# Kernel tuning notes

Measured on AMD Instinct MI355X. Metric: run time of the kernel, lower is better.

Reference implementation:

```python
import jax, jax.numpy as jnp
import numpy as np

NEG_INF = -1e9

def apply_rope(x, positions, head_dim, theta):
    # x: [B, S, H, Dh]; positions: [S] int32
    half = head_dim // 2
    fraction = (2.0 / head_dim) * jnp.arange(half, dtype=jnp.float32)  # [Dh/2]
    timescale = theta ** fraction
    angle = positions.astype(jnp.float32)[:, None] / timescale  # [S, Dh/2]
    sin = jnp.sin(angle)[None, :, None, :]  # [1,S,1,Dh/2]
    cos = jnp.cos(angle)[None, :, None, :]
    x1, x2 = jnp.split(x, 2, axis=-1)
    out = jnp.concatenate([x1 * cos - x2 * sin, x2 * cos + x1 * sin], axis=-1)
    return out.astype(x.dtype)

def setup_inputs() -> dict:
    key = jax.random.key(0)
    B, S, D = 2, 2048, 2048
    Q, N, H = 16, 4, 128
    ks = jax.random.split(key, 5)
    scale = 1.0 / np.sqrt(D)
    return {
        "x": jax.random.normal(ks[0], (B, S, D), dtype=jnp.float32),
        "positions": jnp.arange(S, dtype=jnp.int32),
        "Wq": jax.random.normal(ks[1], (Q, D, H), dtype=jnp.float32) * scale,
        "Wk": jax.random.normal(ks[2], (N, D, H), dtype=jnp.float32) * scale,
        "Wv": jax.random.normal(ks[3], (N, D, H), dtype=jnp.float32) * scale,
        "Wo": jax.random.normal(ks[4], (Q, H, D), dtype=jnp.float32) * scale,
    }

def reference(x, positions, Wq, Wk, Wv, Wo):
    head_dim = Wq.shape[-1]
    theta = 10000.0
    head_repeats = Wq.shape[0] // Wk.shape[0]  # GQA repeat factor

    q_BSQH = jnp.einsum('BSD,QDH->BSQH', x, Wq)
    q_BSQH = apply_rope(q_BSQH, positions, head_dim, theta)
    k_BTNH = jnp.einsum('BSD,NDH->BSNH', x, Wk)
    k_BTNH = apply_rope(k_BTNH, positions, head_dim, theta)
    v_BTNH = jnp.einsum('BSD,NDH->BSNH', x, Wv)

    k_BTQH = jnp.repeat(k_BTNH, head_repeats, axis=2)
    v_BTQH = jnp.repeat(v_BTNH, head_repeats, axis=2)

    scores_BQST = jnp.einsum('BSQH,BTQH->BQST', q_BSQH, k_BTQH) / jnp.sqrt(
        jnp.asarray(head_dim, dtype=x.dtype))
    S = q_BSQH.shape[1]
    causal = jnp.tril(jnp.ones((1, 1, S, S), dtype=jnp.bool_))
    scores_BQST = jnp.where(causal, scores_BQST, NEG_INF)
    weights_BQST = jax.nn.softmax(scores_BQST, axis=-1)
    out_BSQH = jnp.einsum('BQST,BTQH->BSQH', weights_BQST, v_BTQH)
    o_BSD = jnp.einsum('BSQH,QHD->BSD', out_BSQH, Wo)
    return o_BSD
```

## Files before the change

kernel.cpp:

```cpp
#include <hip/hip_runtime.h>
#include <math.h>

#define BB 2
#define SS 2048
#define DD 2048
#define QH 16
#define NKV 4
#define HD 128
#define REP 4
#define NEG_INF_F (-1e9f)

typedef __bf16 bfrag __attribute__((ext_vector_type(8)));
typedef float  ffrag __attribute__((ext_vector_type(4)));

__device__ inline unsigned short f2bf(float f) {
    unsigned u = __builtin_bit_cast(unsigned, f);
    u += 0x7fff + ((u >> 16) & 1);
    return (unsigned short)(u >> 16);
}
__device__ inline float bf2f(unsigned short u) {
    unsigned v = (unsigned)u << 16;
    return __builtin_bit_cast(float, v);
}
__device__ inline bfrag ld_frag(const unsigned short* p) {
    uint4 u = *(const uint4*)p;
    return __builtin_bit_cast(bfrag, u);
}
__device__ inline void async16(const void* g, void* l) {
    __builtin_amdgcn_global_load_lds(
        (const __attribute__((address_space(1))) unsigned int*)g,
        (__attribute__((address_space(3))) unsigned int*)l, 16, 0, 0);
}
__device__ inline unsigned pkbf(float a, float b) {
    unsigned short ua = __builtin_bit_cast(unsigned short, (__bf16)a);
    unsigned short ub = __builtin_bit_cast(unsigned short, (__bf16)b);
    return (unsigned)ua | ((unsigned)ub << 16);
}

__global__ void cast_x_kernel(const float* __restrict__ x,
                              unsigned short* __restrict__ xb, int n)
{
    const int i = (blockIdx.x * blockDim.x + threadIdx.x) * 8;
    if (i >= n) return;
    float4 a = *(const float4*)(x + i);
    float4 b = *(const float4*)(x + i + 4);
    unsigned short o[8];
    o[0] = f2bf(a.x); o[1] = f2bf(a.y); o[2] = f2bf(a.z); o[3] = f2bf(a.w);
    o[4] = f2bf(b.x); o[5] = f2bf(b.y); o[6] = f2bf(b.z); o[7] = f2bf(b.w);
    *(uint4*)(xb + i) = *(uint4*)o;
}

__global__ __launch_bounds__(256) void tcast_kernel(
    const float* __restrict__ in, unsigned short* __restrict__ out,
    int R, int C)
{
    __shared__ float tile[32][33];
    const size_t bofs = (size_t)blockIdx.z * R * C;
    in  += bofs;
    out += bofs;
    const int c0 = blockIdx.x * 32, r0 = blockIdx.y * 32;
    const int tx = threadIdx.x & 31, ty = threadIdx.x >> 5;
    #pragma unroll
    for (int k = 0; k < 4; ++k)
        tile[ty + 8 * k][tx] = in[(size_t)(r0 + ty + 8 * k) * C + c0 + tx];
    __syncthreads();
    #pragma unroll
    for (int k = 0; k < 4; ++k)
        out[(size_t)(c0 + ty + 8 * k) * R + r0 + tx] =
            f2bf(tile[tx][ty + 8 * k]);
}

__global__ __launch_bounds__(256) void gemm_bt_kernel(
    const unsigned short* __restrict__ A,
    const unsigned short* __restrict__ Bt,
    unsigned short* __restrict__ q_out, unsigned short* __restrict__ k_out,
    unsigned short* __restrict__ vt_out, float* __restrict__ f_out,
    int mode)
{
    const int m0 = blockIdx.x * 128;
    const int n0 = blockIdx.y * 128;
    const int tid  = threadIdx.x;
    const int w    = tid >> 6, lane = tid & 63;
    const int l16  = lane & 15, quad = lane >> 4;
    const int wm = (w >> 1) * 64, wn = (w & 1) * 64;

    __shared__ unsigned short As[128 * 32];
    __shared__ unsigned short Bs[128 * 32];

    ffrag acc[4][4];
    #pragma unroll
    for (int mi = 0; mi < 4; ++mi)
        #pragma unroll
        for (int ni = 0; ni < 4; ++ni)
            acc[mi][ni] = (ffrag){0.f, 0.f, 0.f, 0.f};

    for (int k0 = 0; k0 < 2048; k0 += 32) {
        __syncthreads();
        #pragma unroll
        for (int j = 0; j < 2; ++j) {
            const int i   = (j * 4 + w) * 64 + lane;
            const int row = i >> 2, seg = i & 3;
            async16(&A [(size_t)(m0 + row) * 2048 + k0 + seg * 8],
                    (char*)As + i * 16);
            async16(&Bt[(size_t)(n0 + row) * 2048 + k0 + seg * 8],
                    (char*)Bs + i * 16);
        }
        __syncthreads();

        bfrag af[4], bfr[4];
        #pragma unroll
        for (int mi = 0; mi < 4; ++mi)
            af[mi] = ld_frag(&As[(wm + mi * 16 + l16) * 32 + quad * 8]);
        #pragma unroll
        for (int ni = 0; ni < 4; ++ni)
            bfr[ni] = ld_frag(&Bs[(wn + ni * 16 + l16) * 32 + quad * 8]);
        #pragma unroll
        for (int mi = 0; mi < 4; ++mi)
            #pragma unroll
            for (int ni = 0; ni < 4; ++ni)
                acc[mi][ni] = __builtin_amdgcn_mfma_f32_16x16x32_bf16(
                    af[mi], bfr[ni], acc[mi][ni], 0, 0, 0);
    }

    if (mode == 0) {
        #pragma unroll
        for (int mi = 0; mi < 4; ++mi)
            #pragma unroll
            for (int ni = 0; ni < 4; ++ni) {
                const int col = n0 + wn + ni * 16 + l16;
                #pragma unroll
                for (int r = 0; r < 4; ++r) {
                    const int row = m0 + wm + mi * 16 + quad * 4 + r;
                    f_out[(size_t)row * 2048 + col] = acc[mi][ni][r];
                }
            }
    } else if (n0 < 2560) {
        unsigned short* dst;
        int colbase, stride;
        if (n0 < 2048)      { dst = q_out; colbase = n0;        stride = 2048; }
        else                { dst = k_out; colbase = n0 - 2048; stride = 512;  }
        #pragma unroll
        for (int mi = 0; mi < 4; ++mi)
            #pragma unroll
            for (int ni = 0; ni < 4; ++ni) {
                const int col = colbase + wn + ni * 16 + l16;
                #pragma unroll
                for (int r = 0; r < 4; ++r) {
                    const int row = m0 + wm + mi * 16 + quad * 4 + r;
                    dst[(size_t)row * stride + col] = f2bf(acc[mi][ni][r]);
                }
            }
    } else {
        const int c3 = n0 - 2560;
        #pragma unroll
        for (int mi = 0; mi < 4; ++mi)
            #pragma unroll
            for (int ni = 0; ni < 4; ++ni) {
                const int col = c3 + wn + ni * 16 + l16;
                const int nh = col >> 7, h = col & 127;
                const int row0 = m0 + wm + mi * 16 + quad * 4;
                const int b = row0 >> 11, s = row0 & 2047;
                unsigned short pk[4];
                #pragma unroll
                for (int r = 0; r < 4; ++r) pk[r] = f2bf(acc[mi][ni][r]);
                *(uint2*)&vt_out[(((size_t)b * NKV + nh) * HD + h) * SS + s] =
                    *(uint2*)pk;
            }
    }
}

__global__ void rope_kernel(unsigned short* __restrict__ q,
                            unsigned short* __restrict__ k,
                            const int* __restrict__ positions)
{
    const int qpairs = BB * SS * QH * 64;
    const int kpairs = BB * SS * NKV * 64;
    int idx = blockIdx.x * blockDim.x + threadIdx.x;
    unsigned short* base;
    int nh;
    if (idx < qpairs) { base = q; nh = QH; }
    else {
        idx -= qpairs;
        if (idx >= kpairs) return;
        base = k; nh = NKV;
    }
    const int hh   = idx & 63;
    const int rest = idx >> 6;
    const int head = rest % nh;
    const int bs   = rest / nh;
    const int s    = bs % SS;

    unsigned short* p = base + ((size_t)bs * nh + head) * HD;
    const float pos = (float)positions[s];
    const float inv_ts = powf(10000.0f, -(float)hh * (1.0f / 64.0f));
    const float angle = pos * inv_ts;
    const float sn = sinf(angle), cs = cosf(angle);
    const float sc_ = (nh == QH) ? 0.08838834764831845f : 1.0f;
    const float x1 = bf2f(p[hh]), x2 = bf2f(p[hh + 64]);
    p[hh]      = f2bf((x1 * cs - x2 * sn) * sc_);
    p[hh + 64] = f2bf((x2 * cs + x1 * sn) * sc_);
}

__global__ __launch_bounds__(256, 2) void attn_kernel(
    const unsigned short* __restrict__ qb,
    const unsigned short* __restrict__ kb,
    const unsigned short* __restrict__ vt,
    unsigned short* __restrict__ o)
{
    const int bh = blockIdx.y;
    const int b  = bh / QH, qh = bh % QH;
    const int n  = qh / REP;

    const int tid  = threadIdx.x;
    const int w    = tid >> 6;
    const int lane = tid & 63;
    const int l16  = lane & 15;
    const int quad = lane >> 4;
    const int sw   = l16 & 7;

    __shared__ unsigned short Ks[2][2][64][64];
    __shared__ unsigned short Vs[2][128][64];
    __shared__ unsigned short Ps[4][16][72];

    const unsigned short* kbase = kb + (size_t)b * (SS * NKV * HD) + n * HD;
    const unsigned short* vbase = vt + ((size_t)b * NKV + n) * HD * SS;

    for (int ph = 0; ph < 2; ++ph) {
        const int tile = ph == 0 ? (31 - (int)blockIdx.x) : (int)blockIdx.x;
        const int s0 = tile * 64;
        const int rbase = s0 + w * 16 + quad * 4;
        const int thr   = w * 16 + l16;

        bfrag qf[4];
        {
            const unsigned short* qp =
                qb + ((size_t)(b * SS + s0 + w * 16 + l16) * QH + qh) * HD
                   + quad * 8;
            #pragma unroll
            for (int c = 0; c < 4; ++c) qf[c] = ld_frag(qp + c * 32);
        }
        ffrag oacc[8];
        #pragma unroll
        for (int t = 0; t < 8; ++t) oacc[t] = (ffrag){0.f, 0.f, 0.f, 0.f};
        float mr = -1e30f, lr = 0.0f;

        #pragma unroll
        for (int j = 0; j < 4; ++j) {
            const int s = j * 256 + tid;
            {   const int cc = s >> 9, t = (s >> 3) & 63;
                const int sl = (s & 7) ^ (t & 7);
                async16(kbase + (size_t)t * (NKV * HD) + cc * 64 + sl * 8,
                        (char*)&Ks[0][0][0][0] + s * 16);
            }
            {   const int h = s >> 3, sl = (s & 7) ^ (h & 7);
                async16(vbase + (size_t)h * SS + sl * 8,
                        (char*)&Vs[0][0][0] + s * 16);
            }
        }
        __syncthreads();

        int p = 0;
        for (int t0 = 0; t0 <= s0; t0 += 64, p ^= 1) {
            if (t0 + 64 <= s0) {
                const int tn = t0 + 64;
                #pragma unroll
                for (int j = 0; j < 4; ++j) {
                    const int s = j * 256 + tid;
                    {   const int cc = s >> 9, t = (s >> 3) & 63;
                        const int sl = (s & 7) ^ (t & 7);
                        async16(kbase + (size_t)(tn + t) * (NKV * HD)
                                      + cc * 64 + sl * 8,
                                (char*)&Ks[p ^ 1][0][0][0] + s * 16);
                    }
                    {   const int h = s >> 3, sl = (s & 7) ^ (h & 7);
                        async16(vbase + (size_t)h * SS + tn + sl * 8,
                                (char*)&Vs[p ^ 1][0][0] + s * 16);
                    }
                }
            }

            ffrag sc[4];
            #pragma unroll
            for (int t = 0; t < 4; ++t) sc[t] = (ffrag){0.f, 0.f, 0.f, 0.f};
            #pragma unroll
            for (int c = 0; c < 4; ++c) {
                const int cc = c >> 1, cb = (c & 1) * 4;
                #pragma unroll
                for (int t = 0; t < 4; ++t) {
                    bfrag kfr = ld_frag(
                        &Ks[p][cc][t * 16 + l16][((cb + quad) ^ sw) * 8]);
                    sc[t] = __builtin_amdgcn_mfma_f32_16x16x32_bf16(
                        kfr, qf[c], sc[t], 0, 0, 0);
                }
            }

            const bool diag = (t0 == s0);
            if (diag) {
                #pragma unroll
                for (int t = 0; t < 4; ++t) {
                    const int col0 = t * 16 + quad * 4;
                    #pragma unroll
                    for (int r = 0; r < 4; ++r)
                        if (col0 + r > thr) sc[t][r] = NEG_INF_F;
                }
            }

            float tmax;
            {
                float a0 = fmaxf(fmaxf(sc[0][0], sc[0][1]),
                                 fmaxf(sc[0][2], sc[0][3]));
                float a1 = fmaxf(fmaxf(sc[1][0], sc[1][1]),
                                 fmaxf(sc[1][2], sc[1][3]));
                float a2 = fmaxf(fmaxf(sc[2][0], sc[2][1]),
                                 fmaxf(sc[2][2], sc[2][3]));
                float a3 = fmaxf(fmaxf(sc[3][0], sc[3][1]),
                                 fmaxf(sc[3][2], sc[3][3]));
                tmax = fmaxf(fmaxf(a0, a1), fmaxf(a2, a3));
            }
            tmax = fmaxf(tmax, __shfl_xor(tmax, 16));
            tmax = fmaxf(tmax, __shfl_xor(tmax, 32));

            if (__any(tmax > mr + 8.0f)) {
                const float mnew  = fmaxf(mr, tmax);
                const float alpha = __expf(mr - mnew);
                lr *= alpha;
                mr = mnew;
                #pragma unroll
                for (int r = 0; r < 4; ++r) {
                    const float ar =
                        __shfl(alpha, (lane & 48) | (quad * 4 + r));
                    #pragma unroll
                    for (int t = 0; t < 8; ++t) oacc[t][r] *= ar;
                }
            }

            float ps = 0.f;
            #pragma unroll
            for (int t = 0; t < 4; ++t) {
                const float p0 = __expf(sc[t][0] - mr);
                const float p1 = __expf(sc[t][1] - mr);
                const float p2 = __expf(sc[t][2] - mr);
                const float p3 = __expf(sc[t][3] - mr);
                ps += (p0 + p1) + (p2 + p3);
                uint2 pk2;
                pk2.x = pkbf(p0, p1);
                pk2.y = pkbf(p2, p3);
                *(uint2*)&Ps[w][l16][t * 16 + quad * 4] = pk2;
            }
            ps += __shfl_xor(ps, 16);
            ps += __shfl_xor(ps, 32);
            lr += ps;

            #pragma unroll
            for (int c = 0; c < 2; ++c) {
                bfrag pf = ld_frag(&Ps[w][l16][c * 32 + quad * 8]);
                #pragma unroll
                for (int t = 0; t < 8; ++t) {
                    bfrag vf = ld_frag(
                        &Vs[p][t * 16 + l16][((c * 4 + quad) ^ sw) * 8]);
                    oacc[t] = __builtin_amdgcn_mfma_f32_16x16x32_bf16(
                        pf, vf, oacc[t], 0, 0, 0);
                }
            }

            __syncthreads();
        }

        #pragma unroll
        for (int r = 0; r < 4; ++r) {
            const float lrr  = __shfl(lr, (lane & 48) | (quad * 4 + r));
            const float invl = 1.0f / lrr;
            const int row = rbase + r;
            unsigned short* op = o + ((size_t)(b * SS + row) * QH + qh) * HD;
            #pragma unroll
            for (int t = 0; t < 8; ++t)
                op[t * 16 + l16] = f2bf(oacc[t][r] * invl);
        }
    }
}

extern "C" void kernel_launch(void* const* d_in, const int* in_sizes, int n_in,
                              void* d_out, int out_size, void* d_ws,
                              size_t ws_size, hipStream_t stream)
{
    const float* x         = (const float*)d_in[0];
    const int*   positions = (const int*)d_in[1];
    const float* Wq        = (const float*)d_in[2];
    const float* Wk        = (const float*)d_in[3];
    const float* Wv        = (const float*)d_in[4];
    const float* Wo        = (const float*)d_in[5];
    float* out = (float*)d_out;

    char* ws = (char*)d_ws;
    unsigned short* xb    = (unsigned short*)ws;
    unsigned short* Wqkvt = (unsigned short*)(ws + (16u << 20));
    unsigned short* Wot   = (unsigned short*)(ws + (28u << 20));
    unsigned short* qbf   = (unsigned short*)(ws + (36u << 20));
    unsigned short* kbf   = (unsigned short*)(ws + (52u << 20));
    unsigned short* vtb   = (unsigned short*)(ws + (56u << 20));
    unsigned short* opre  = xb;

    const int nx = BB * SS * DD;
    cast_x_kernel<<<nx / (8 * 256), 256, 0, stream>>>(x, xb, nx);

    tcast_kernel<<<dim3(4, 64, 16), 256, 0, stream>>>(Wq, Wqkvt, 2048, 128);
    tcast_kernel<<<dim3(4, 64, 4), 256, 0, stream>>>(
        Wk, Wqkvt + (size_t)16 * 128 * 2048, 2048, 128);
    tcast_kernel<<<dim3(4, 64, 4), 256, 0, stream>>>(
        Wv, Wqkvt + (size_t)20 * 128 * 2048, 2048, 128);
    tcast_kernel<<<dim3(64, 64, 1), 256, 0, stream>>>(Wo, Wot, 2048, 2048);

    gemm_bt_kernel<<<dim3(32, 24), 256, 0, stream>>>(
        xb, Wqkvt, qbf, kbf, vtb, nullptr, 1);

    const int pairs = BB * SS * (QH + NKV) * 64;
    rope_kernel<<<(pairs + 255) / 256, 256, 0, stream>>>(qbf, kbf, positions);

    dim3 g2(16, BB * QH);
    attn_kernel<<<g2, 256, 0, stream>>>(qbf, kbf, vtb, opre);

    gemm_bt_kernel<<<dim3(32, 16), 256, 0, stream>>>(
        opre, Wot, nullptr, nullptr, nullptr, out, 0);
}
```

Measured before the change: 360.9 us.

## Double-buffer GEMM LDS, swizzle tiles, remap blocks across XCDs, raise MFMA priority

The projection GEMM now double-buffers its LDS tiles, issuing the async load for the next K slice before computing the current one. It also XOR-swizzles the LDS layout to cut bank conflicts on fragment reads. Both GEMM and attention block indices are remapped so consecutive logical tiles spread round-robin across the 8 XCDs for better L2 locality. The attention MFMA sections are wrapped in s_setprio to favour matrix issue over other waves. Costs are doubled GEMM LDS use, which may lower occupancy, and a remap that assumes the grid size is divisible by 8.

```diff
diff --git a/kernel.cpp b/kernel.cpp
--- a/kernel.cpp
+++ b/kernel.cpp
@@ -77,15 +77,21 @@
     unsigned short* __restrict__ vt_out, float* __restrict__ f_out,
     int mode)
 {
-    const int m0 = blockIdx.x * 128;
-    const int n0 = blockIdx.y * 128;
+    const int gy = gridDim.y;
+    int f = blockIdx.x * gy + blockIdx.y;
+    const int chunk = (gridDim.x * gy) >> 3;
+    f = (f & 7) * chunk + (f >> 3);
+    const int m0 = (f / gy) * 128;
+    const int n0 = (f % gy) * 128;
+
     const int tid  = threadIdx.x;
     const int w    = tid >> 6, lane = tid & 63;
     const int l16  = lane & 15, quad = lane >> 4;
     const int wm = (w >> 1) * 64, wn = (w & 1) * 64;
-
-    __shared__ unsigned short As[128 * 32];
-    __shared__ unsigned short Bs[128 * 32];
+    const int sl4 = l16 & 3;
+
+    __shared__ unsigned short As[2][128 * 32];
+    __shared__ unsigned short Bs[2][128 * 32];
 
     ffrag acc[4][4];
     #pragma unroll
@@ -94,32 +100,43 @@
         for (int ni = 0; ni < 4; ++ni)
             acc[mi][ni] = (ffrag){0.f, 0.f, 0.f, 0.f};
 
-    for (int k0 = 0; k0 < 2048; k0 += 32) {
-        __syncthreads();
+    auto stage = [&](int b, int k0) {
         #pragma unroll
         for (int j = 0; j < 2; ++j) {
             const int i   = (j * 4 + w) * 64 + lane;
-            const int row = i >> 2, seg = i & 3;
-            async16(&A [(size_t)(m0 + row) * 2048 + k0 + seg * 8],
-                    (char*)As + i * 16);
-            async16(&Bt[(size_t)(n0 + row) * 2048 + k0 + seg * 8],
-                    (char*)Bs + i * 16);
+            const int row = i >> 2;
+            const int sl  = (i & 3) ^ (row & 3);
+            async16(&A [(size_t)(m0 + row) * 2048 + k0 + sl * 8],
+                    (char*)&As[b][0] + i * 16);
+            async16(&Bt[(size_t)(n0 + row) * 2048 + k0 + sl * 8],
+                    (char*)&Bs[b][0] + i * 16);
         }
-        __syncthreads();
+    };
+
+    stage(0, 0);
+    __syncthreads();
+    int cur = 0;
+    for (int k0 = 0; k0 < 2048; k0 += 32) {
+        if (k0 + 32 < 2048) stage(cur ^ 1, k0 + 32);
 
         bfrag af[4], bfr[4];
         #pragma unroll
         for (int mi = 0; mi < 4; ++mi)
-            af[mi] = ld_frag(&As[(wm + mi * 16 + l16) * 32 + quad * 8]);
+            af[mi] = ld_frag(
+                &As[cur][(wm + mi * 16 + l16) * 32 + (quad ^ sl4) * 8]);
         #pragma unroll
         for (int ni = 0; ni < 4; ++ni)
-            bfr[ni] = ld_frag(&Bs[(wn + ni * 16 + l16) * 32 + quad * 8]);
+            bfr[ni] = ld_frag(
+                &Bs[cur][(wn + ni * 16 + l16) * 32 + (quad ^ sl4) * 8]);
         #pragma unroll
         for (int mi = 0; mi < 4; ++mi)
             #pragma unroll
             for (int ni = 0; ni < 4; ++ni)
                 acc[mi][ni] = __builtin_amdgcn_mfma_f32_16x16x32_bf16(
                     af[mi], bfr[ni], acc[mi][ni], 0, 0, 0);
+
+        __syncthreads();
+        cur ^= 1;
     }
 
     if (mode == 0) {
@@ -207,7 +224,11 @@
     const unsigned short* __restrict__ vt,
     unsigned short* __restrict__ o)
 {
-    const int bh = blockIdx.y;
+    int f = blockIdx.y * 16 + blockIdx.x;
+    f = (f & 7) * 64 + (f >> 3);
+    const int bh = f >> 4;
+    const int bx = f & 15;
+
     const int b  = bh / QH, qh = bh % QH;
     const int n  = qh / REP;
 
@@ -226,7 +247,7 @@
     const unsigned short* vbase = vt + ((size_t)b * NKV + n) * HD * SS;
 
     for (int ph = 0; ph < 2; ++ph) {
-        const int tile = ph == 0 ? (31 - (int)blockIdx.x) : (int)blockIdx.x;
+        const int tile = ph == 0 ? (31 - bx) : bx;
         const int s0 = tile * 64;
         const int rbase = s0 + w * 16 + quad * 4;
         const int thr   = w * 16 + l16;
@@ -282,6 +303,7 @@
             ffrag sc[4];
             #pragma unroll
             for (int t = 0; t < 4; ++t) sc[t] = (ffrag){0.f, 0.f, 0.f, 0.f};
+            __builtin_amdgcn_s_setprio(1);
             #pragma unroll
             for (int c = 0; c < 4; ++c) {
                 const int cc = c >> 1, cb = (c & 1) * 4;
@@ -293,6 +315,7 @@
                         kfr, qf[c], sc[t], 0, 0, 0);
                 }
             }
+            __builtin_amdgcn_s_setprio(0);
 
             const bool diag = (t0 == s0);
             if (diag) {
@@ -351,6 +374,7 @@
             ps += __shfl_xor(ps, 32);
             lr += ps;
 
+            __builtin_amdgcn_s_setprio(1);
             #pragma unroll
             for (int c = 0; c < 2; ++c) {
                 bfrag pf = ld_frag(&Ps[w][l16][c * 32 + quad * 8]);
@@ -362,6 +386,7 @@
                         pf, vf, oacc[t], 0, 0, 0);
                 }
             }
+            __builtin_amdgcn_s_setprio(0);
 
             __syncthreads();
         }
```

Result: no change. 361.0 us (+0.0%).

## Fuse prep casts into one kernel and widen attention blocks to 128-query tiles

Applied to the files above, without the earlier changes.

Merges the x cast and the four weight transpose-casts into a single launch to cut launch overhead. The attention kernel moves to 512 threads handling 128 query rows per block, so each K/V tile loaded into LDS is shared by twice as many waves. It also remaps the block order, swizzles the P scratch buffer to avoid LDS bank conflicts, and raises wave priority around the MFMA sections. The cost is more register and LDS pressure per block, and waves in the lower half idle on the last diagonal tile.

```diff
diff --git a/kernel.cpp b/kernel.cpp
--- a/kernel.cpp
+++ b/kernel.cpp
@@ -37,29 +37,50 @@
     return (unsigned)ua | ((unsigned)ub << 16);
 }
 
-__global__ void cast_x_kernel(const float* __restrict__ x,
-                              unsigned short* __restrict__ xb, int n)
-{
-    const int i = (blockIdx.x * blockDim.x + threadIdx.x) * 8;
-    if (i >= n) return;
-    float4 a = *(const float4*)(x + i);
-    float4 b = *(const float4*)(x + i + 4);
-    unsigned short o[8];
-    o[0] = f2bf(a.x); o[1] = f2bf(a.y); o[2] = f2bf(a.z); o[3] = f2bf(a.w);
-    o[4] = f2bf(b.x); o[5] = f2bf(b.y); o[6] = f2bf(b.z); o[7] = f2bf(b.w);
-    *(uint4*)(xb + i) = *(uint4*)o;
-}
-
-__global__ __launch_bounds__(256) void tcast_kernel(
-    const float* __restrict__ in, unsigned short* __restrict__ out,
-    int R, int C)
+__global__ __launch_bounds__(256) void prep_kernel(
+    const float* __restrict__ x, unsigned short* __restrict__ xb,
+    const float* __restrict__ Wq, const float* __restrict__ Wk,
+    const float* __restrict__ Wv, const float* __restrict__ Wo,
+    unsigned short* __restrict__ Wqkvt, unsigned short* __restrict__ Wot)
 {
     __shared__ float tile[32][33];
-    const size_t bofs = (size_t)blockIdx.z * R * C;
-    in  += bofs;
-    out += bofs;
-    const int c0 = blockIdx.x * 32, r0 = blockIdx.y * 32;
-    const int tx = threadIdx.x & 31, ty = threadIdx.x >> 5;
+    const int blk = blockIdx.x;
+    const int tid = threadIdx.x;
+
+    if (blk < 4096) {
+        const int i = blk * 2048 + tid * 8;
+        float4 a = *(const float4*)(x + i);
+        float4 b = *(const float4*)(x + i + 4);
+        unsigned short o[8];
+        o[0] = f2bf(a.x); o[1] = f2bf(a.y); o[2] = f2bf(a.z); o[3] = f2bf(a.w);
+        o[4] = f2bf(b.x); o[5] = f2bf(b.y); o[6] = f2bf(b.z); o[7] = f2bf(b.w);
+        *(uint4*)(xb + i) = *(uint4*)o;
+        return;
+    }
+
+    const float* in;
+    unsigned short* out;
+    int R, C, bx, by;
+    if (blk < 10240) {
+        const int lw = blk - 4096;
+        const int z  = lw >> 8;
+        const int r  = lw & 255;
+        bx = r & 3; by = r >> 2;
+        R = 2048; C = 128;
+        if (z < 16)      { in = Wq + (size_t)z * 2048 * 128;
+                           out = Wqkvt + (size_t)z * 128 * 2048; }
+        else if (z < 20) { in = Wk + (size_t)(z - 16) * 2048 * 128;
+                           out = Wqkvt + (size_t)(16 + (z - 16)) * 128 * 2048; }
+        else             { in = Wv + (size_t)(z - 20) * 2048 * 128;
+                           out = Wqkvt + (size_t)(20 + (z - 20)) * 128 * 2048; }
+    } else {
+        const int lw = blk - 10240;
+        bx = lw & 63; by = lw >> 6;
+        R = 2048; C = 2048;
+        in = Wo; out = Wot;
+    }
+    const int c0 = bx * 32, r0 = by * 32;
+    const int tx = tid & 31, ty = tid >> 5;
     #pragma unroll
     for (int k = 0; k < 4; ++k)
         tile[ty + 8 * k][tx] = in[(size_t)(r0 + ty + 8 * k) * C + c0 + tx];
@@ -201,13 +222,17 @@
     p[hh + 64] = f2bf((x2 * cs + x1 * sn) * sc_);
 }
 
-__global__ __launch_bounds__(256, 2) void attn_kernel(
+__global__ __launch_bounds__(512, 4) void attn_kernel(
     const unsigned short* __restrict__ qb,
     const unsigned short* __restrict__ kb,
     const unsigned short* __restrict__ vt,
     unsigned short* __restrict__ o)
 {
-    const int bh = blockIdx.y;
+    int f = blockIdx.y * 8 + blockIdx.x;
+    f = (f & 7) * 32 + (f >> 3);
+    const int bh = f >> 3;
+    const int bx = f & 7;
+
     const int b  = bh / QH, qh = bh % QH;
     const int n  = qh / REP;
 
@@ -220,16 +245,17 @@
 
     __shared__ unsigned short Ks[2][2][64][64];
     __shared__ unsigned short Vs[2][128][64];
-    __shared__ unsigned short Ps[4][16][72];
+    __shared__ unsigned short Ps[8][16][64];
 
     const unsigned short* kbase = kb + (size_t)b * (SS * NKV * HD) + n * HD;
     const unsigned short* vbase = vt + ((size_t)b * NKV + n) * HD * SS;
 
     for (int ph = 0; ph < 2; ++ph) {
-        const int tile = ph == 0 ? (31 - (int)blockIdx.x) : (int)blockIdx.x;
-        const int s0 = tile * 64;
+        const int super = ph == 0 ? (15 - bx) : bx;
+        const int s0    = super * 128;
         const int rbase = s0 + w * 16 + quad * 4;
-        const int thr   = w * 16 + l16;
+        const int thr   = s0 + w * 16 + l16;
+        const int dlim  = s0 + ((w >> 2) << 6);
 
         bfrag qf[4];
         {
@@ -245,8 +271,8 @@
         float mr = -1e30f, lr = 0.0f;
 
         #pragma unroll
-        for (int j = 0; j < 4; ++j) {
-            const int s = j * 256 + tid;
+        for (int j = 0; j < 2; ++j) {
+            const int s = j * 512 + tid;
             {   const int cc = s >> 9, t = (s >> 3) & 63;
                 const int sl = (s & 7) ^ (t & 7);
                 async16(kbase + (size_t)t * (NKV * HD) + cc * 64 + sl * 8,
@@ -260,12 +286,12 @@
         __syncthreads();
 
         int p = 0;
-        for (int t0 = 0; t0 <= s0; t0 += 64, p ^= 1) {
-            if (t0 + 64 <= s0) {
+        for (int t0 = 0; t0 <= s0 + 64; t0 += 64, p ^= 1) {
+            if (t0 <= s0) {
                 const int tn = t0 + 64;
                 #pragma unroll
-                for (int j = 0; j < 4; ++j) {
-                    const int s = j * 256 + tid;
+                for (int j = 0; j < 2; ++j) {
+                    const int s = j * 512 + tid;
                     {   const int cc = s >> 9, t = (s >> 3) & 63;
                         const int sl = (s & 7) ^ (t & 7);
                         async16(kbase + (size_t)(tn + t) * (NKV * HD)
@@ -279,88 +305,96 @@
                 }
             }
 
-            ffrag sc[4];
-            #pragma unroll
-            for (int t = 0; t < 4; ++t) sc[t] = (ffrag){0.f, 0.f, 0.f, 0.f};
-            #pragma unroll
-            for (int c = 0; c < 4; ++c) {
-                const int cc = c >> 1, cb = (c & 1) * 4;
+            if (t0 <= dlim) {
+                ffrag sc[4];
+                #pragma unroll
+                for (int t = 0; t < 4; ++t)
+                    sc[t] = (ffrag){0.f, 0.f, 0.f, 0.f};
+                __builtin_amdgcn_s_setprio(1);
+                #pragma unroll
+                for (int c = 0; c < 4; ++c) {
+                    const int cc = c >> 1, cb = (c & 1) * 4;
+                    #pragma unroll
+                    for (int t = 0; t < 4; ++t) {
+                        bfrag kfr = ld_frag(
+                            &Ks[p][cc][t * 16 + l16][((cb + quad) ^ sw) * 8]);
+                        sc[t] = __builtin_amdgcn_mfma_f32_16x16x32_bf16(
+                            kfr, qf[c], sc[t], 0, 0, 0);
+                    }
+                }
+                __builtin_amdgcn_s_setprio(0);
+
+                if (t0 == dlim) {
+                    #pragma unroll
+                    for (int t = 0; t < 4; ++t) {
+                        const int col0 = t0 + t * 16 + quad * 4;
+                        #pragma unroll
+                        for (int r = 0; r < 4; ++r)
+                            if (col0 + r > thr) sc[t][r] = NEG_INF_F;
+                    }
+                }
+
+                float tmax;
+                {
+                    float a0 = fmaxf(fmaxf(sc[0][0], sc[0][1]),
+                                     fmaxf(sc[0][2], sc[0][3]));
+                    float a1 = fmaxf(fmaxf(sc[1][0], sc[1][1]),
+                                     fmaxf(sc[1][2], sc[1][3]));
+                    float a2 = fmaxf(fmaxf(sc[2][0], sc[2][1]),
+                                     fmaxf(sc[2][2], sc[2][3]));
+                    float a3 = fmaxf(fmaxf(sc[3][0], sc[3][1]),
+                                     fmaxf(sc[3][2], sc[3][3]));
+                    tmax = fmaxf(fmaxf(a0, a1), fmaxf(a2, a3));
+                }
+                tmax = fmaxf(tmax, __shfl_xor(tmax, 16));
+                tmax = fmaxf(tmax, __shfl_xor(tmax, 32));
+
+                if (__any(tmax > mr + 8.0f)) {
+                    const float mnew  = fmaxf(mr, tmax);
+                    const float alpha = __expf(mr - mnew);
+                    lr *= alpha;
+                    mr = mnew;
+                    #pragma unroll
+                    for (int r = 0; r < 4; ++r) {
+                        const float ar =
+                            __shfl(alpha, (lane & 48) | (quad * 4 + r));
+                        #pragma unroll
+                        for (int t = 0; t < 8; ++t) oacc[t][r] *= ar;
+                    }
+                }
+
+                float ps = 0.f;
                 #pragma unroll
                 for (int t = 0; t < 4; ++t) {
-                    bfrag kfr = ld_frag(
-                        &Ks[p][cc][t * 16 + l16][((cb + quad) ^ sw) * 8]);
-                    sc[t] = __builtin_amdgcn_mfma_f32_16x16x32_bf16(
-                        kfr, qf[c], sc[t], 0, 0, 0);
-                }
-            }
-
-            const bool diag = (t0 == s0);
-            if (diag) {
-                #pragma unroll
-                for (int t = 0; t < 4; ++t) {
-                    const int col0 = t * 16 + quad * 4;
+                    const float p0 = __expf(sc[t][0] - mr);
+                    const float p1 = __expf(sc[t][1] - mr);
+                    const float p2 = __expf(sc[t][2] - mr);
+                    const float p3 = __expf(sc[t][3] - mr);
+                    ps += (p0 + p1) + (p2 + p3);
+                    uint2 pk2;
+                    pk2.x = pkbf(p0, p1);
+                    pk2.y = pkbf(p2, p3);
+                    const int sl = (2 * t + (quad >> 1)) ^ sw;
+                    *(uint2*)&Ps[w][l16][sl * 8 + (quad & 1) * 4] = pk2;
+                }
+                ps += __shfl_xor(ps, 16);
+                ps += __shfl_xor(ps, 32);
+                lr += ps;
+
+                __builtin_amdgcn_s_setprio(1);
+                #pragma unroll
+                for (int c = 0; c < 2; ++c) {
+                    bfrag pf = ld_frag(
+                        &Ps[w][l16][((c * 4 + quad) ^ sw) * 8]);
                     #pragma unroll
-                    for (int r = 0; r < 4; ++r)
-                        if (col0 + r > thr) sc[t][r] = NEG_INF_F;
-                }
-            }
-
-            float tmax;
-            {
-                float a0 = fmaxf(fmaxf(sc[0][0], sc[0][1]),
-                                 fmaxf(sc[0][2], sc[0][3]));
-                float a1 = fmaxf(fmaxf(sc[1][0], sc[1][1]),
-                                 fmaxf(sc[1][2], sc[1][3]));
-                float a2 = fmaxf(fmaxf(sc[2][0], sc[2][1]),
-                                 fmaxf(sc[2][2], sc[2][3]));
-                float a3 = fmaxf(fmaxf(sc[3][0], sc[3][1]),
-                                 fmaxf(sc[3][2], sc[3][3]));
-                tmax = fmaxf(fmaxf(a0, a1), fmaxf(a2, a3));
-            }
-            tmax = fmaxf(tmax, __shfl_xor(tmax, 16));
-            tmax = fmaxf(tmax, __shfl_xor(tmax, 32));
-
-            if (__any(tmax > mr + 8.0f)) {
-                const float mnew  = fmaxf(mr, tmax);
-                const float alpha = __expf(mr - mnew);
-                lr *= alpha;
-                mr = mnew;
-                #pragma unroll
-                for (int r = 0; r < 4; ++r) {
-                    const float ar =
-                        __shfl(alpha, (lane & 48) | (quad * 4 + r));
-                    #pragma unroll
-                    for (int t = 0; t < 8; ++t) oacc[t][r] *= ar;
-                }
-            }
-
-            float ps = 0.f;
-            #pragma unroll
-            for (int t = 0; t < 4; ++t) {
-                const float p0 = __expf(sc[t][0] - mr);
-                const float p1 = __expf(sc[t][1] - mr);
-                const float p2 = __expf(sc[t][2] - mr);
-                const float p3 = __expf(sc[t][3] - mr);
-                ps += (p0 + p1) + (p2 + p3);
-                uint2 pk2;
-                pk2.x = pkbf(p0, p1);
-                pk2.y = pkbf(p2, p3);
-                *(uint2*)&Ps[w][l16][t * 16 + quad * 4] = pk2;
-            }
-            ps += __shfl_xor(ps, 16);
-            ps += __shfl_xor(ps, 32);
-            lr += ps;
-
-            #pragma unroll
-            for (int c = 0; c < 2; ++c) {
-                bfrag pf = ld_frag(&Ps[w][l16][c * 32 + quad * 8]);
-                #pragma unroll
-                for (int t = 0; t < 8; ++t) {
-                    bfrag vf = ld_frag(
-                        &Vs[p][t * 16 + l16][((c * 4 + quad) ^ sw) * 8]);
-                    oacc[t] = __builtin_amdgcn_mfma_f32_16x16x32_bf16(
-                        pf, vf, oacc[t], 0, 0, 0);
-                }
+                    for (int t = 0; t < 8; ++t) {
+                        bfrag vf = ld_frag(
+                            &Vs[p][t * 16 + l16][((c * 4 + quad) ^ sw) * 8]);
+                        oacc[t] = __builtin_amdgcn_mfma_f32_16x16x32_bf16(
+                            pf, vf, oacc[t], 0, 0, 0);
+                    }
+                }
+                __builtin_amdgcn_s_setprio(0);
             }
 
             __syncthreads();
@@ -400,15 +434,7 @@
     unsigned short* vtb   = (unsigned short*)(ws + (56u << 20));
     unsigned short* opre  = xb;
 
-    const int nx = BB * SS * DD;
-    cast_x_kernel<<<nx / (8 * 256), 256, 0, stream>>>(x, xb, nx);
-
-    tcast_kernel<<<dim3(4, 64, 16), 256, 0, stream>>>(Wq, Wqkvt, 2048, 128);
-    tcast_kernel<<<dim3(4, 64, 4), 256, 0, stream>>>(
-        Wk, Wqkvt + (size_t)16 * 128 * 2048, 2048, 128);
-    tcast_kernel<<<dim3(4, 64, 4), 256, 0, stream>>>(
-        Wv, Wqkvt + (size_t)20 * 128 * 2048, 2048, 128);
-    tcast_kernel<<<dim3(64, 64, 1), 256, 0, stream>>>(Wo, Wot, 2048, 2048);
+    prep_kernel<<<14336, 256, 0, stream>>>(x, xb, Wq, Wk, Wv, Wo, Wqkvt, Wot);
 
     gemm_bt_kernel<<<dim3(32, 24), 256, 0, stream>>>(
         xb, Wqkvt, qbf, kbf, vtb, nullptr, 1);
@@ -416,8 +442,8 @@
     const int pairs = BB * SS * (QH + NKV) * 64;
     rope_kernel<<<(pairs + 255) / 256, 256, 0, stream>>>(qbf, kbf, positions);
 
-    dim3 g2(16, BB * QH);
-    attn_kernel<<<g2, 256, 0, stream>>>(qbf, kbf, vtb, opre);
+    dim3 g2(8, BB * QH);
+    attn_kernel<<<g2, 512, 0, stream>>>(qbf, kbf, vtb, opre);
 
     gemm_bt_kernel<<<dim3(32, 16), 256, 0, stream>>>(
         opre, Wot, nullptr, nullptr, nullptr, out, 0);
```

Result: no change. 365.0 us (+1.1%).
